# Kernel optimization log

Hardware: AMD Instinct MI355X
Metric: run time of the kernel (lower is better)

The kernel has to match this reference:

```python
import jax, jax.numpy as jnp
import numpy as np

N_NODES = 100000
N_EDGES = 3200000
FEATURE = 128
HIDDEN = 128
N_LAYERS = 3


def _glorot(key, fan_in, fan_out):
    lim = np.sqrt(6.0 / (fan_in + fan_out)).astype(np.float32)
    return jax.random.uniform(key, (fan_in, fan_out), jnp.float32, -lim, lim)


def setup_inputs() -> dict:
    key = jax.random.key(0)
    ks = jax.random.split(key, 8)
    x = jax.random.normal(ks[0], (N_NODES, FEATURE), jnp.float32)
    edge_index = jax.random.randint(ks[1], (2, N_EDGES), 0, N_NODES, jnp.int64)
    W0 = _glorot(ks[2], FEATURE, HIDDEN)
    W1 = _glorot(ks[3], HIDDEN, HIDDEN)
    W2 = _glorot(ks[4], HIDDEN, HIDDEN)
    b0 = jnp.zeros((HIDDEN,), jnp.float32)
    b1 = jnp.zeros((HIDDEN,), jnp.float32)
    b2 = jnp.zeros((HIDDEN,), jnp.float32)
    return {"x": x, "edge_index": edge_index,
            "W0": W0, "b0": b0, "W1": W1, "b1": b1, "W2": W2, "b2": b2}


def _gcn_conv(x, W, b, src, dst, n):
    # PyG GCNConv: linear -> add self loops -> sym-norm aggregate -> +bias
    h = x @ W  # [N, H]
    loop = jnp.arange(n)
    s = jnp.concatenate([src, loop])  # sources incl. self loops
    d = jnp.concatenate([dst, loop])  # targets incl. self loops
    deg = jax.ops.segment_sum(jnp.ones_like(d, dtype=h.dtype), d, num_segments=n)
    dinv = jnp.where(deg > 0, jax.lax.rsqrt(jnp.maximum(deg, 1.0)), 0.0)
    norm = dinv[s] * dinv[d]  # [E+N]
    out = jax.ops.segment_sum(h[s] * norm[:, None], d, num_segments=n)
    return out + b


def reference(x, edge_index, W0, b0, W1, b1, W2, b2):
    # forward of GCN: (GCNConv -> relu -> dropout[eval=no-op]) x layer
    src, dst = edge_index[0], edge_index[1]
    n = x.shape[0]
    for W, b in ((W0, b0), (W1, b1), (W2, b2)):
        x = jax.nn.relu(_gcn_conv(x, W, b, src, dst, n))
    return x
```

## Files before the change

### kernel.cpp

```cpp
#include <hip/hip_runtime.h>
#include <hip/hip_fp16.h>

#define N_NODES 100000
#define N_EDGES 3200000
#define NBUCKETS 391
#define NCHUNKB 512
#define CHUNK 6250

typedef __attribute__((ext_vector_type(8))) short sh8;
typedef __attribute__((ext_vector_type(4))) float fl4;

__device__ inline void split_bf16(float x, short& hi, short& lo) {
    unsigned u = __float_as_uint(x);
    unsigned r = u + 0x7FFFu + ((u >> 16) & 1u);
    hi = (short)(r >> 16);
    float hif = __uint_as_float(r & 0xFFFF0000u);
    float lof = x - hif;
    unsigned u2 = __float_as_uint(lof);
    lo = (short)((u2 + 0x7FFFu + ((u2 >> 16) & 1u)) >> 16);
}


__global__ __launch_bounds__(512) void k_bzero(int* __restrict__ bucket_cnt) {
    int t = threadIdx.x;
    if (t < NBUCKETS) bucket_cnt[t] = 0;
}

__global__ __launch_bounds__(256) void k_bhist(const int* __restrict__ ei_dst,
                                               int* __restrict__ bucket_cnt) {
    __shared__ int h[NBUCKETS];
    int t = threadIdx.x;
    for (int i = t; i < NBUCKETS; i += 256) h[i] = 0;
    __syncthreads();
    int base = blockIdx.x * CHUNK;
    for (int i = t; i < CHUNK; i += 256)
        atomicAdd(&h[ei_dst[base + i] >> 8], 1);
    __syncthreads();
    for (int i = t; i < NBUCKETS; i += 256)
        if (h[i]) atomicAdd(&bucket_cnt[i], h[i]);
}

__global__ __launch_bounds__(512) void k_bscan(const int* __restrict__ bucket_cnt,
                                               int* __restrict__ bucket_base,
                                               int* __restrict__ bucket_fill) {
    __shared__ int s[512];
    int t = threadIdx.x;
    int v = (t < NBUCKETS) ? bucket_cnt[t] : 0;
    s[t] = v;
    __syncthreads();
    for (int off = 1; off < 512; off <<= 1) {
        int x = (t >= off) ? s[t - off] : 0;
        __syncthreads();
        s[t] += x;
        __syncthreads();
    }
    int ex = s[t] - v;
    if (t < NBUCKETS) { bucket_base[t] = ex; bucket_fill[t] = ex; }
    if (t == NBUCKETS - 1) bucket_base[NBUCKETS] = s[t];
}

__global__ __launch_bounds__(256) void k_bscatter(const int* __restrict__ ei,
                                                  int* __restrict__ bucket_fill,
                                                  unsigned* __restrict__ bpairs) {
    __shared__ int h[NBUCKETS];
    __shared__ int basep[NBUCKETS];
    int t = threadIdx.x;
    const int* dstp = ei + N_EDGES;
    int base = blockIdx.x * CHUNK;

    for (int i = t; i < NBUCKETS; i += 256) h[i] = 0;
    __syncthreads();
    for (int i = t; i < CHUNK; i += 256)
        atomicAdd(&h[dstp[base + i] >> 8], 1);
    __syncthreads();
    for (int i = t; i < NBUCKETS; i += 256) {
        int c = h[i];
        basep[i] = c ? atomicAdd(&bucket_fill[i], c) : 0;
    }
    __syncthreads();
    for (int i = t; i < NBUCKETS; i += 256) h[i] = 0;
    __syncthreads();
    for (int i = t; i < CHUNK; i += 256) {
        int d = dstp[base + i];
        int s = ei[base + i];
        int b = d >> 8;
        int r = atomicAdd(&h[b], 1);
        bpairs[basep[b] + r] = (unsigned)s | ((unsigned)(d & 255) << 17);
    }
}

__global__ __launch_bounds__(256) void k_bbuild(const unsigned* __restrict__ bpairs,
                                                const int* __restrict__ bucket_base,
                                                int* __restrict__ row_ptr,
                                                int* __restrict__ cnt,
                                                float* __restrict__ dinv,
                                                int* __restrict__ csr_src) {
    __shared__ int h[256];
    __shared__ int sc[256];
    int b = blockIdx.x;
    int t = threadIdx.x;
    int e0 = bucket_base[b], e1 = bucket_base[b + 1];

    h[t] = 0;
    __syncthreads();
    for (int i = e0 + t; i < e1; i += 256)
        atomicAdd(&h[bpairs[i] >> 17], 1);
    __syncthreads();
    int v = h[t];
    sc[t] = v;
    __syncthreads();
    for (int off = 1; off < 256; off <<= 1) {
        int x = (t >= off) ? sc[t - off] : 0;
        __syncthreads();
        sc[t] += x;
        __syncthreads();
    }
    int ex = sc[t] - v;
    int node = b * 256 + t;
    if (node < N_NODES) {
        cnt[node] = v;
        dinv[node] = rsqrtf((float)(v + 1));
        row_ptr[node] = e0 + ex;
    }
    __syncthreads();
    h[t] = e0 + ex;
    __syncthreads();
    for (int i = e0 + t; i < e1; i += 256) {
        unsigned p = bpairs[i];
        int pos = atomicAdd(&h[p >> 17], 1);
        csr_src[pos] = (int)(p & 0x1FFFFu);
    }
}


__global__ __launch_bounds__(256) void k_wprep(const float* __restrict__ W0,
                                               const float* __restrict__ W1,
                                               const float* __restrict__ W2,
                                               short* __restrict__ fhi,
                                               short* __restrict__ flo) {
    int idx = blockIdx.x * 256 + threadIdx.x;
    int l = idx >> 14, e = idx & 16383;
    const float* W = (l == 0) ? W0 : (l == 1) ? W1 : W2;
    float w = W[e];
    int k = e >> 7, n = e & 127;
    int ks = k >> 5, q = (k >> 3) & 3, j = k & 7;
    int c = n >> 4, n16 = n & 15;
    int lane = q * 16 + n16;
    int dst = ((l * 32 + ks * 8 + c) * 64 + lane) * 8 + j;
    short hi, lo;
    split_bf16(w, hi, lo);
    fhi[dst] = hi;
    flo[dst] = lo;
}


__global__ __launch_bounds__(256, 3) void k_gemm_mfma(const float* __restrict__ X,
                                                      const short* __restrict__ fhi,
                                                      const short* __restrict__ flo,
                                                      const float* __restrict__ dinv,
                                                      __half* __restrict__ H16) {
    int t = threadIdx.x;
    int wave = t >> 6, lane = t & 63;
    int q = lane >> 4, n16 = lane & 15;
    int tile = blockIdx.x * 4 + wave;
    int row_base = tile * 16;

    int r0 = row_base + n16;
    if (r0 > N_NODES - 1) r0 = N_NODES - 1;
    const float* p0 = X + (long long)r0 * 128 + q * 8;
    float4 a[4][2];
#pragma unroll
    for (int ks = 0; ks < 4; ++ks) {
        a[ks][0] = *(const float4*)(p0 + ks * 32);
        a[ks][1] = *(const float4*)(p0 + ks * 32 + 4);
    }

    sh8 ah[4], al[4];
#pragma unroll
    for (int ks = 0; ks < 4; ++ks) {
        float xs[8];
        xs[0] = a[ks][0].x; xs[1] = a[ks][0].y; xs[2] = a[ks][0].z; xs[3] = a[ks][0].w;
        xs[4] = a[ks][1].x; xs[5] = a[ks][1].y; xs[6] = a[ks][1].z; xs[7] = a[ks][1].w;
#pragma unroll
        for (int j = 0; j < 8; ++j) {
            short h, l;
            split_bf16(xs[j], h, l);
            ah[ks][j] = h;
            al[ks][j] = l;
        }
    }

    const sh8* __restrict__ BH = (const sh8*)fhi;
    const sh8* __restrict__ BL = (const sh8*)flo;

    fl4 acc[8];
#pragma unroll
    for (int c = 0; c < 8; ++c) acc[c] = (fl4){0.f, 0.f, 0.f, 0.f};

#pragma unroll
    for (int ks = 0; ks < 4; ++ks) {
        sh8 bh[8], bl[8];
#pragma unroll
        for (int c = 0; c < 8; ++c) {
            bh[c] = BH[(ks * 8 + c) * 64 + lane];
            bl[c] = BL[(ks * 8 + c) * 64 + lane];
        }
#pragma unroll
        for (int c = 0; c < 8; ++c) {
            acc[c] = __builtin_amdgcn_mfma_f32_16x16x32_bf16(ah[ks], bh[c], acc[c], 0, 0, 0);
            acc[c] = __builtin_amdgcn_mfma_f32_16x16x32_bf16(al[ks], bh[c], acc[c], 0, 0, 0);
            acc[c] = __builtin_amdgcn_mfma_f32_16x16x32_bf16(ah[ks], bl[c], acc[c], 0, 0, 0);
        }
    }

#pragma unroll
    for (int reg = 0; reg < 4; ++reg) {
        int grow = row_base + q * 4 + reg;
        if (grow < N_NODES) {
            float sc = dinv[grow];
            __half* dst = H16 + (long long)grow * 128 + n16;
#pragma unroll
            for (int c = 0; c < 8; ++c)
                dst[c * 16] = __float2half(acc[c][reg] * sc);
        }
    }
}


__global__ __launch_bounds__(256) void k_gather(const __half2* __restrict__ H2,
                                                const int* __restrict__ csr_src,
                                                const int* __restrict__ row_ptr,
                                                const int* __restrict__ cnt,
                                                const float* __restrict__ dinv,
                                                const float* __restrict__ b,
                                                float* __restrict__ out) {
    int wv = __builtin_amdgcn_readfirstlane(threadIdx.x >> 6);
    int node = blockIdx.x * 4 + wv;
    int lane = threadIdx.x & 63;
    if (node >= N_NODES) return;

    int start = row_ptr[node];
    int n = cnt[node];

    float2 self_ = __half22float2(H2[node * 64 + lane]);
    float accx = self_.x, accy = self_.y;

    int j = 0;
    for (; j + 8 <= n; j += 8) {
        int s[8];
#pragma unroll
        for (int u = 0; u < 8; ++u) s[u] = csr_src[start + j + u];
        float2 h[8];
#pragma unroll
        for (int u = 0; u < 8; ++u) h[u] = __half22float2(H2[s[u] * 64 + lane]);
#pragma unroll
        for (int u = 0; u < 8; ++u) { accx += h[u].x; accy += h[u].y; }
    }
    for (; j < n; ++j) {
        float2 h = __half22float2(H2[csr_src[start + j] * 64 + lane]);
        accx += h.x; accy += h.y;
    }

    float dd = dinv[node];
    float2 bb = ((const float2*)b)[lane];
    float2 v;
    v.x = fmaxf(fmaf(accx, dd, bb.x), 0.0f);
    v.y = fmaxf(fmaf(accy, dd, bb.y), 0.0f);
    ((float2*)out)[node * 64 + lane] = v;
}


extern "C" void kernel_launch(void* const* d_in, const int* in_sizes, int n_in,
                              void* d_out, int out_size, void* d_ws, size_t ws_size,
                              hipStream_t stream) {
    const float* x  = (const float*)d_in[0];
    const int*   ei = (const int*)d_in[1];
    const float* Wm[3] = {(const float*)d_in[2], (const float*)d_in[4], (const float*)d_in[6]};
    const float* bv[3] = {(const float*)d_in[3], (const float*)d_in[5], (const float*)d_in[7]};
    float* out = (float*)d_out;

    char* w = (char*)d_ws;
    int*      row_ptr     = (int*)(w + 0);
    int*      cnt         = (int*)(w + 400384);
    float*    dinv        = (float*)(w + 800768);
    int*      bucket_cnt  = (int*)(w + 1201152);
    int*      bucket_base = (int*)(w + 1203200);
    int*      bucket_fill = (int*)(w + 1205248);
    unsigned* bpairs      = (unsigned*)(w + 1207296);
    int*      csr_src     = (int*)(w + 14007808);
    short*    fragHi      = (short*)(w + 26808320);
    short*    fragLo      = (short*)(w + 26906624);
    __half*   H16         = (__half*)(w + 27004928);

    k_bzero<<<1, 512, 0, stream>>>(bucket_cnt);
    k_bhist<<<NCHUNKB, 256, 0, stream>>>(ei + N_EDGES, bucket_cnt);
    k_bscan<<<1, 512, 0, stream>>>(bucket_cnt, bucket_base, bucket_fill);
    k_bscatter<<<NCHUNKB, 256, 0, stream>>>(ei, bucket_fill, bpairs);
    k_bbuild<<<NBUCKETS, 256, 0, stream>>>(bpairs, bucket_base, row_ptr, cnt, dinv, csr_src);
    k_wprep<<<192, 256, 0, stream>>>(Wm[0], Wm[1], Wm[2], fragHi, fragLo);

    const float* xin = x;
    for (int l = 0; l < 3; ++l) {
        k_gemm_mfma<<<1563, 256, 0, stream>>>(xin, fragHi + l * 16384, fragLo + l * 16384,
                                              dinv, H16);
        k_gather<<<(N_NODES + 3) / 4, 256, 0, stream>>>((const __half2*)H16, csr_src,
                                                        row_ptr, cnt, dinv, bv[l], out);
        xin = out;
    }
}
```

Measured before the change: 624.8 us.

## Stage weight fragments in LDS for GEMM and fold bucket zeroing into wprep

The GEMM kernel now uses 512-thread blocks of 8 waves covering 128 rows. Each block copies the hi/lo bf16 weight fragments (64 KB) into shared memory once, and all waves read B from LDS instead of re-reading it from global memory per wave. The separate bucket-zeroing kernel is merged into an extra block of k_wprep to remove one launch, and the histogram/scatter chunk count is halved. The 64 KB LDS footprint per block may limit occupancy, and the edge-sorting kernels get fewer, larger blocks.

```diff
diff --git a/kernel.cpp b/kernel.cpp
--- a/kernel.cpp
+++ b/kernel.cpp
@@ -4,8 +4,8 @@
 #define N_NODES 100000
 #define N_EDGES 3200000
 #define NBUCKETS 391
-#define NCHUNKB 512
-#define CHUNK 6250
+#define NCHUNKB 256
+#define CHUNK 12500
 
 typedef __attribute__((ext_vector_type(8))) short sh8;
 typedef __attribute__((ext_vector_type(4))) float fl4;
@@ -20,11 +20,6 @@
     lo = (short)((u2 + 0x7FFFu + ((u2 >> 16) & 1u)) >> 16);
 }
 
-
-__global__ __launch_bounds__(512) void k_bzero(int* __restrict__ bucket_cnt) {
-    int t = threadIdx.x;
-    if (t < NBUCKETS) bucket_cnt[t] = 0;
-}
 
 __global__ __launch_bounds__(256) void k_bhist(const int* __restrict__ ei_dst,
                                                int* __restrict__ bucket_cnt) {
@@ -137,7 +132,12 @@
                                                const float* __restrict__ W1,
                                                const float* __restrict__ W2,
                                                short* __restrict__ fhi,
-                                               short* __restrict__ flo) {
+                                               short* __restrict__ flo,
+                                               int* __restrict__ bucket_cnt) {
+    if (blockIdx.x == 192) {
+        for (int i = threadIdx.x; i < NBUCKETS; i += 256) bucket_cnt[i] = 0;
+        return;
+    }
     int idx = blockIdx.x * 256 + threadIdx.x;
     int l = idx >> 14, e = idx & 16383;
     const float* W = (l == 0) ? W0 : (l == 1) ? W1 : W2;
@@ -154,16 +154,18 @@
 }
 
 
-__global__ __launch_bounds__(256, 3) void k_gemm_mfma(const float* __restrict__ X,
+__global__ __launch_bounds__(512, 4) void k_gemm_mfma(const float* __restrict__ X,
                                                       const short* __restrict__ fhi,
                                                       const short* __restrict__ flo,
                                                       const float* __restrict__ dinv,
                                                       __half* __restrict__ H16) {
+    __shared__ short Bh[16384];
+    __shared__ short Bl[16384];
+
     int t = threadIdx.x;
     int wave = t >> 6, lane = t & 63;
     int q = lane >> 4, n16 = lane & 15;
-    int tile = blockIdx.x * 4 + wave;
-    int row_base = tile * 16;
+    int row_base = blockIdx.x * 128 + wave * 16;
 
     int r0 = row_base + n16;
     if (r0 > N_NODES - 1) r0 = N_NODES - 1;
@@ -173,6 +175,18 @@
     for (int ks = 0; ks < 4; ++ks) {
         a[ks][0] = *(const float4*)(p0 + ks * 32);
         a[ks][1] = *(const float4*)(p0 + ks * 32 + 4);
+    }
+
+    {
+        const float4* sh_ = (const float4*)fhi;
+        const float4* sl_ = (const float4*)flo;
+        float4* dh = (float4*)Bh;
+        float4* dl = (float4*)Bl;
+#pragma unroll
+        for (int i = 0; i < 4; ++i) {
+            dh[t + i * 512] = sh_[t + i * 512];
+            dl[t + i * 512] = sl_[t + i * 512];
+        }
     }
 
     sh8 ah[4], al[4];
@@ -190,28 +204,22 @@
         }
     }
 
-    const sh8* __restrict__ BH = (const sh8*)fhi;
-    const sh8* __restrict__ BL = (const sh8*)flo;
-
     fl4 acc[8];
 #pragma unroll
     for (int c = 0; c < 8; ++c) acc[c] = (fl4){0.f, 0.f, 0.f, 0.f};
 
-#pragma unroll
-    for (int ks = 0; ks < 4; ++ks) {
-        sh8 bh[8], bl[8];
+    __syncthreads();
+
+#pragma unroll
+    for (int ks = 0; ks < 4; ++ks)
 #pragma unroll
         for (int c = 0; c < 8; ++c) {
-            bh[c] = BH[(ks * 8 + c) * 64 + lane];
-            bl[c] = BL[(ks * 8 + c) * 64 + lane];
+            sh8 bh = *(const sh8*)&Bh[((ks * 8 + c) * 64 + lane) * 8];
+            sh8 bl = *(const sh8*)&Bl[((ks * 8 + c) * 64 + lane) * 8];
+            acc[c] = __builtin_amdgcn_mfma_f32_16x16x32_bf16(ah[ks], bh, acc[c], 0, 0, 0);
+            acc[c] = __builtin_amdgcn_mfma_f32_16x16x32_bf16(al[ks], bh, acc[c], 0, 0, 0);
+            acc[c] = __builtin_amdgcn_mfma_f32_16x16x32_bf16(ah[ks], bl, acc[c], 0, 0, 0);
         }
-#pragma unroll
-        for (int c = 0; c < 8; ++c) {
-            acc[c] = __builtin_amdgcn_mfma_f32_16x16x32_bf16(ah[ks], bh[c], acc[c], 0, 0, 0);
-            acc[c] = __builtin_amdgcn_mfma_f32_16x16x32_bf16(al[ks], bh[c], acc[c], 0, 0, 0);
-            acc[c] = __builtin_amdgcn_mfma_f32_16x16x32_bf16(ah[ks], bl[c], acc[c], 0, 0, 0);
-        }
-    }
 
 #pragma unroll
     for (int reg = 0; reg < 4; ++reg) {
@@ -292,17 +300,16 @@
     short*    fragLo      = (short*)(w + 26906624);
     __half*   H16         = (__half*)(w + 27004928);
 
-    k_bzero<<<1, 512, 0, stream>>>(bucket_cnt);
+    k_wprep<<<193, 256, 0, stream>>>(Wm[0], Wm[1], Wm[2], fragHi, fragLo, bucket_cnt);
     k_bhist<<<NCHUNKB, 256, 0, stream>>>(ei + N_EDGES, bucket_cnt);
     k_bscan<<<1, 512, 0, stream>>>(bucket_cnt, bucket_base, bucket_fill);
     k_bscatter<<<NCHUNKB, 256, 0, stream>>>(ei, bucket_fill, bpairs);
     k_bbuild<<<NBUCKETS, 256, 0, stream>>>(bpairs, bucket_base, row_ptr, cnt, dinv, csr_src);
-    k_wprep<<<192, 256, 0, stream>>>(Wm[0], Wm[1], Wm[2], fragHi, fragLo);
 
     const float* xin = x;
     for (int l = 0; l < 3; ++l) {
-        k_gemm_mfma<<<1563, 256, 0, stream>>>(xin, fragHi + l * 16384, fragLo + l * 16384,
-                                              dinv, H16);
+        k_gemm_mfma<<<(N_NODES + 127) / 128, 512, 0, stream>>>(xin, fragHi + l * 16384,
+                                                               fragLo + l * 16384, dinv, H16);
         k_gather<<<(N_NODES + 3) / 4, 256, 0, stream>>>((const __half2*)H16, csr_src,
                                                         row_ptr, cnt, dinv, bv[l], out);
         xin = out;
```

After: 594.1 us. 4.9% less time.
